# Kernel optimization log

Hardware: AMD Instinct MI355X
Metric: run time of the kernel (lower is better)

The kernel has to match this reference:

```python
import jax, jax.numpy as jnp
import numpy as np
from jax import lax

N, T, D_DYN = 3000, 64, 5
POP, DEMO, ECO, R = 16, 32, 16, 128
SLOPE = 0.01  # torch LeakyReLU default


def _leaky(x):
    return jnp.where(x >= 0, x, SLOPE * x)


def setup_inputs() -> dict:
    key = jax.random.key(0)
    ks = jax.random.split(key, 30)
    rn = lambda k, shape, s=0.1: (jax.random.normal(k, shape, jnp.float32) * s)
    inp = {
        "dynamic": jax.random.normal(ks[0], (N, T, D_DYN), jnp.float32),
        "pop": jax.random.normal(ks[1], (N, POP), jnp.float32),
        "demo": jax.random.normal(ks[2], (N, DEMO), jnp.float32),
        "eco": jax.random.normal(ks[3], (N, ECO), jnp.float32),
        "geo": jax.random.normal(ks[4], (N * N, 2), jnp.float32),
        # GAT-style static attention params
        "W_pop": rn(ks[5], (POP, POP)), "a_pop": rn(ks[6], (2 * POP, 1)),
        "W_demo": rn(ks[7], (DEMO, DEMO)), "a_demo": rn(ks[8], (2 * DEMO, 1)),
        "W_eco": rn(ks[9], (ECO, ECO)), "a_eco": rn(ks[10], (2 * ECO, 1)),
        "W_geo": rn(ks[11], (2, 2)), "a_geo": rn(ks[12], (2, 1)),
        # covid_weight MLP: 1 -> R -> 1
        "cw_w1": rn(ks[13], (1, R)), "cw_b1": rn(ks[14], (R,)),
        "cw_w2": rn(ks[15], (R, 1)), "cw_b2": rn(ks[16], (1,)),
        # hos_weight MLP: 4 -> R -> 4
        "hw_w1": rn(ks[17], (4, R)), "hw_b1": rn(ks[18], (R,)),
        "hw_w2": rn(ks[19], (R, 4)), "hw_b2": rn(ks[20], (4,)),
        # LSTM (torch gate order i,f,g,o), combined bias b_ih + b_hh
        "Wih": rn(ks[21], (D_DYN, 4 * R)), "Whh": rn(ks[22], (R, 4 * R)),
        "b_lstm": rn(ks[23], (4 * R,)),
        # output head
        "lin_w": rn(ks[24], (R, R)), "lin_b": rn(ks[25], (R,)),
        "lin2_w": rn(ks[26], (R, 1)), "lin2_b": rn(ks[27], (1,)),
    }
    return inp


def _pair_scores(x, W, a):
    # faithful to sigmoid(cat([h_i, h_j]) @ a): score[i,j] = h_i @ a1 + h_j @ a2
    h = x @ W                       # [N, D]
    d = W.shape[0]
    s1 = h @ a[:d, 0]               # [N]
    s2 = h @ a[d:, 0]               # [N]
    return jax.nn.sigmoid(s1[:, None] + s2[None, :])  # [N, N]


def _lstm(x, Wih, Whh, b):
    # x: [N, T, D_DYN] -> h_seq [N, T, R], (hT, cT)
    n = x.shape[0]
    h0 = jnp.zeros((n, R), x.dtype)
    c0 = jnp.zeros((n, R), x.dtype)

    def step(carry, xt):
        h, c = carry
        z = xt @ Wih + h @ Whh + b          # [N, 4R]
        i, f, g, o = jnp.split(z, 4, axis=-1)
        i, f, o = jax.nn.sigmoid(i), jax.nn.sigmoid(f), jax.nn.sigmoid(o)
        g = jnp.tanh(g)
        c = f * c + i * g
        h = o * jnp.tanh(c)
        return (h, c), h

    (hT, cT), hs = lax.scan(step, (h0, c0), x.transpose(1, 0, 2))
    return hs.transpose(1, 0, 2), hT, cT


def reference(dynamic, pop, demo, eco, geo,
              W_pop, a_pop, W_demo, a_demo, W_eco, a_eco, W_geo, a_geo,
              cw_w1, cw_b1, cw_w2, cw_b2, hw_w1, hw_b1, hw_w2, hw_b2,
              Wih, Whh, b_lstm, lin_w, lin_b, lin2_w, lin2_b):
    n, t = pop.shape[0], dynamic.shape[1]

    d_pop = _pair_scores(pop, W_pop, a_pop)
    d_demo = _pair_scores(demo, W_demo, a_demo)
    d_eco = _pair_scores(eco, W_eco, a_eco)
    d_geo = jax.nn.sigmoid(((geo @ W_geo) @ a_geo).reshape(n, n))

    dist = jax.nn.softmax(d_pop + d_demo + d_eco + d_geo, axis=-1)  # [N, N]

    cov_in = dynamic[:, :, 0:1]                                     # [N, T, 1]
    cov_w = jax.nn.sigmoid(_leaky(cov_in @ cw_w1 + cw_b1) @ cw_w2 + cw_b2)
    hos_in = dynamic[:, :, 1:5]                                     # [N, T, 4]
    hos_w = jax.nn.sigmoid(_leaky(hos_in @ hw_w1 + hw_b1) @ hw_w2 + hw_b2)
    total_weights = jnp.concatenate([cov_w, hos_w], axis=-1)        # [N, T, 5]

    h, hT, cT = _lstm(total_weights * dynamic, Wih, Whh, b_lstm)    # [N, T, R]

    # original: h + (h.reshape(N,1,T,R).repeat(1,N,1,1) * dist[:,:,None,None]).sum(1)
    # == h + h * dist.sum(axis=1) (h is broadcast along the summed axis)
    h_att = h + h * dist.sum(axis=1)[:, None, None]

    y = _leaky(h_att @ lin_w + lin_b) @ lin2_w + lin2_b             # [N, T, 1]
    return (y, dist, total_weights, hT, cT)
```

## Files before the change

kernel.cpp:

```cpp
#include <hip/hip_runtime.h>
#include <hip/hip_bf16.h>

#define N_NODES 3000
#define T_STEPS 64
#define POP     16
#define DEMO    32
#define ECO     16
#define R       128
#define SLOPE   0.01f

#define NBLK    250

#define WS_S1P 0
#define WS_S1D 3000
#define WS_S1E 6000
#define WS_S2P 9000
#define WS_S2D 12000
#define WS_S2E 15000
#define WS_GV  18000
#define WS_ATT 18432
#define WS_XW  21504
#define WS_PACK_F 981504

#define OUT_Y    0
#define OUT_DIST 192000
#define OUT_TW   9192000
#define OUT_HT   10152000
#define OUT_CT   10536000

typedef __bf16 bf16x8 __attribute__((ext_vector_type(8)));
typedef float  f32x4  __attribute__((ext_vector_type(4)));

__device__ __forceinline__ float sigf(float x) {
  return __builtin_amdgcn_rcpf(1.0f + __expf(-x));
}
__device__ __forceinline__ float leakyf(float x) { return x >= 0.0f ? x : SLOPE * x; }
__device__ __forceinline__ float tanhfast(float x) {
  return fmaf(-2.0f, __builtin_amdgcn_rcpf(__expf(2.0f * x) + 1.0f), 1.0f);
}
__device__ __forceinline__ unsigned short bfbits(float v) {
  __bf16 b = (__bf16)v;
  return __builtin_bit_cast(unsigned short, b);
}
template <int CTRL>
__device__ __forceinline__ float dppsum(float v) {
  int p = __builtin_amdgcn_update_dpp(0, __builtin_bit_cast(int, v), CTRL, 0xF, 0xF, true);
  return v + __builtin_bit_cast(float, p);
}

#define PIN4(x) { f32x4 _t = __builtin_bit_cast(f32x4, x); \
                  asm volatile("" : "+v"(_t)); \
                  x = __builtin_bit_cast(bf16x8, _t); }
#define PIN1(x) asm volatile("" : "+v"(x))

__global__ __launch_bounds__(256) void pack_kernel(
    const float* __restrict__ Whh, const float* __restrict__ lin_w,
    const float* __restrict__ Wih, const float* __restrict__ b_lstm,
    unsigned short* __restrict__ wsu)
{
  int idx = blockIdx.x * 256 + threadIdx.x;
  if (idx < 65536) {
    int i = idx & 7, lane = (idx >> 3) & 63, kc = (idx >> 9) & 3, ct = idx >> 11;
    int k = kc * 32 + ((lane >> 4) << 3) + i;
    int n = ct * 16 + (lane & 15);
    float v = Whh[k * 512 + n];
    float hi = (float)(__bf16)v;
    wsu[idx]         = bfbits(v);
    wsu[65536 + idx] = bfbits(v - hi);
  } else if (idx < 81920) {
    int q = idx - 65536;
    int i = q & 7, lane = (q >> 3) & 63, kc = (q >> 9) & 3, ct = q >> 11;
    int k = kc * 32 + ((lane >> 4) << 3) + i;
    int n = ct * 16 + (lane & 15);
    float v = lin_w[k * R + n];
    float hi = (float)(__bf16)v;
    wsu[131072 + q] = bfbits(v);
    wsu[147456 + q] = bfbits(v - hi);
  } else {
    int q = idx - 81920;
    int i = q & 7, lane = (q >> 3) & 63, ct = q >> 9;
    int ks = ((lane >> 4) << 3) + i;
    int n = ct * 16 + (lane & 15);
    unsigned short o = 0;
    if (ks < 5) {
      o = bfbits(Wih[ks * 512 + n]);
    } else if (ks == 6) {
      float b = b_lstm[n];
      o = bfbits(b - (float)(__bf16)b);
    } else if (ks == 7) {
      o = bfbits(b_lstm[n]);
    }
    wsu[163840 + q] = o;
  }
}

__global__ __launch_bounds__(256) void scores_kernel(
    const float* __restrict__ pop,  const float* __restrict__ demo,
    const float* __restrict__ eco,
    const float* __restrict__ W_pop,  const float* __restrict__ a_pop,
    const float* __restrict__ W_demo, const float* __restrict__ a_demo,
    const float* __restrict__ W_eco,  const float* __restrict__ a_eco,
    const float* __restrict__ W_geo,  const float* __restrict__ a_geo,
    float* __restrict__ ws)
{
  int i = blockIdx.x * blockDim.x + threadIdx.x;
  if (i == 0) {
    float a0 = a_geo[0], a1 = a_geo[1];
    ws[WS_GV + 0] = W_geo[0] * a0 + W_geo[1] * a1;
    ws[WS_GV + 1] = W_geo[2] * a0 + W_geo[3] * a1;
  }
  if (i >= N_NODES) return;
  {
    float x[POP];
#pragma unroll
    for (int k = 0; k < POP; k++) x[k] = pop[i * POP + k];
    float s1 = 0.f, s2 = 0.f;
#pragma unroll
    for (int r = 0; r < POP; r++) {
      float h = 0.f;
#pragma unroll
      for (int k = 0; k < POP; k++) h = fmaf(x[k], W_pop[k * POP + r], h);
      s1 = fmaf(h, a_pop[r], s1);
      s2 = fmaf(h, a_pop[POP + r], s2);
    }
    ws[WS_S1P + i] = s1; ws[WS_S2P + i] = s2;
  }
  {
    float x[DEMO];
#pragma unroll
    for (int k = 0; k < DEMO; k++) x[k] = demo[i * DEMO + k];
    float s1 = 0.f, s2 = 0.f;
#pragma unroll 4
    for (int r = 0; r < DEMO; r++) {
      float h = 0.f;
#pragma unroll
      for (int k = 0; k < DEMO; k++) h = fmaf(x[k], W_demo[k * DEMO + r], h);
      s1 = fmaf(h, a_demo[r], s1);
      s2 = fmaf(h, a_demo[DEMO + r], s2);
    }
    ws[WS_S1D + i] = s1; ws[WS_S2D + i] = s2;
  }
  {
    float x[ECO];
#pragma unroll
    for (int k = 0; k < ECO; k++) x[k] = eco[i * ECO + k];
    float s1 = 0.f, s2 = 0.f;
#pragma unroll
    for (int r = 0; r < ECO; r++) {
      float h = 0.f;
#pragma unroll
      for (int k = 0; k < ECO; k++) h = fmaf(x[k], W_eco[k * ECO + r], h);
      s1 = fmaf(h, a_eco[r], s1);
      s2 = fmaf(h, a_eco[ECO + r], s2);
    }
    ws[WS_S1E + i] = s1; ws[WS_S2E + i] = s2;
  }
}

__global__ __launch_bounds__(256) void weights_kernel(
    const float* __restrict__ dyn,
    const float* __restrict__ cw_w1, const float* __restrict__ cw_b1,
    const float* __restrict__ cw_w2, const float* __restrict__ cw_b2,
    const float* __restrict__ hw_w1, const float* __restrict__ hw_b1,
    const float* __restrict__ hw_w2, const float* __restrict__ hw_b2,
    float* __restrict__ out, float* __restrict__ ws)
{
  __shared__ float s_cw1[R], s_cb1[R], s_cw2[R], s_hb1[R];
  __shared__ float s_hw1[4 * R], s_hw2[R * 4];
  int tid = threadIdx.x;
  if (tid < R) {
    s_cw1[tid] = cw_w1[tid]; s_cb1[tid] = cw_b1[tid];
    s_cw2[tid] = cw_w2[tid]; s_hb1[tid] = hw_b1[tid];
  }
  for (int i = tid; i < 4 * R; i += 256) { s_hw1[i] = hw_w1[i]; s_hw2[i] = hw_w2[i]; }
  __syncthreads();

  int idx = blockIdx.x * 256 + tid;
  float x0 = dyn[idx * 5 + 0], x1 = dyn[idx * 5 + 1], x2 = dyn[idx * 5 + 2];
  float x3 = dyn[idx * 5 + 3], x4 = dyn[idx * 5 + 4];

  float acc = 0.f, o0 = 0.f, o1 = 0.f, o2 = 0.f, o3 = 0.f;
#pragma unroll 8
  for (int r = 0; r < R; r++) {
    float u = leakyf(fmaf(x0, s_cw1[r], s_cb1[r]));
    acc = fmaf(u, s_cw2[r], acc);
    float v = s_hb1[r];
    v = fmaf(x1, s_hw1[r], v);
    v = fmaf(x2, s_hw1[R + r], v);
    v = fmaf(x3, s_hw1[2 * R + r], v);
    v = fmaf(x4, s_hw1[3 * R + r], v);
    v = leakyf(v);
    o0 = fmaf(v, s_hw2[r * 4 + 0], o0);
    o1 = fmaf(v, s_hw2[r * 4 + 1], o1);
    o2 = fmaf(v, s_hw2[r * 4 + 2], o2);
    o3 = fmaf(v, s_hw2[r * 4 + 3], o3);
  }
  float tw0 = sigf(acc + cw_b2[0]);
  float tw1 = sigf(o0 + hw_b2[0]);
  float tw2 = sigf(o1 + hw_b2[1]);
  float tw3 = sigf(o2 + hw_b2[2]);
  float tw4 = sigf(o3 + hw_b2[3]);

  out[OUT_TW + idx * 5 + 0] = tw0;
  out[OUT_TW + idx * 5 + 1] = tw1;
  out[OUT_TW + idx * 5 + 2] = tw2;
  out[OUT_TW + idx * 5 + 3] = tw3;
  out[OUT_TW + idx * 5 + 4] = tw4;

  ws[WS_XW + idx * 5 + 0] = tw0 * x0;
  ws[WS_XW + idx * 5 + 1] = tw1 * x1;
  ws[WS_XW + idx * 5 + 2] = tw2 * x2;
  ws[WS_XW + idx * 5 + 3] = tw3 * x3;
  ws[WS_XW + idx * 5 + 4] = tw4 * x4;
}

__global__ __launch_bounds__(256) void dist_kernel(
    const float* __restrict__ geo, float* __restrict__ out, float* __restrict__ ws)
{
  int i = blockIdx.x;
  int tid = threadIdx.x;
  __shared__ float sm[20];

  float s1p = ws[WS_S1P + i], s1d = ws[WS_S1D + i], s1e = ws[WS_S1E + i];
  float gv0 = ws[WS_GV + 0], gv1 = ws[WS_GV + 1];

  float vals[12];
  float vmax = -3.0e38f;
#pragma unroll
  for (int u = 0; u < 12; u++) {
    int j = tid + u * 256;
    float v = -3.0e38f;
    if (j < N_NODES) {
      float2 g = *(const float2*)&geo[((size_t)i * N_NODES + j) * 2];
      v = sigf(s1p + ws[WS_S2P + j]) + sigf(s1d + ws[WS_S2D + j]) +
          sigf(s1e + ws[WS_S2E + j]) + sigf(fmaf(g.x, gv0, g.y * gv1));
    }
    vals[u] = v;
    vmax = fmaxf(vmax, v);
  }
  int wid = tid >> 6, lane = tid & 63;
  for (int off = 32; off; off >>= 1) vmax = fmaxf(vmax, __shfl_down(vmax, off, 64));
  if (lane == 0) sm[wid] = vmax;
  __syncthreads();
  if (tid == 0) sm[8] = fmaxf(fmaxf(sm[0], sm[1]), fmaxf(sm[2], sm[3]));
  __syncthreads();
  vmax = sm[8];

  float lsum = 0.f;
#pragma unroll
  for (int u = 0; u < 12; u++) {
    int j = tid + u * 256;
    float e = (j < N_NODES) ? __expf(vals[u] - vmax) : 0.f;
    vals[u] = e;
    lsum += e;
  }
  for (int off = 32; off; off >>= 1) lsum += __shfl_down(lsum, off, 64);
  if (lane == 0) sm[4 + wid] = lsum;
  __syncthreads();
  if (tid == 0) sm[9] = sm[4] + sm[5] + sm[6] + sm[7];
  __syncthreads();
  float inv = __builtin_amdgcn_rcpf(sm[9]);

  float rs = 0.f;
#pragma unroll
  for (int u = 0; u < 12; u++) {
    int j = tid + u * 256;
    if (j < N_NODES) {
      float wv = vals[u] * inv;
      out[OUT_DIST + (size_t)i * N_NODES + j] = wv;
      rs += wv;
    }
  }
  for (int off = 32; off; off >>= 1) rs += __shfl_down(rs, off, 64);
  if (lane == 0) sm[10 + wid] = rs;
  __syncthreads();
  if (tid == 0) ws[WS_ATT + i] = 1.0f + (sm[10] + sm[11] + sm[12] + sm[13]);
}

#define HB        6144
#define XWH       4096
#define XWL       5120
#define PART_OFF  12288
#define LDS_BYTES 13312

__global__ __launch_bounds__(512, 2) void lstm_kernel(
    const unsigned short* __restrict__ wsu,
    const float* __restrict__ ws,
    const float* __restrict__ lin_b, const float* __restrict__ lin2_w,
    const float* __restrict__ lin2_b,
    float* __restrict__ out)
{
  __shared__ __align__(16) char smraw[LDS_BYTES];
  float* PARTf = (float*)(smraw + PART_OFF);
  int tid = threadIdx.x;
  int w = tid >> 6, lane = tid & 63;
  int lg = lane >> 4, lc = lane & 15;
  int row0 = blockIdx.x * 12;

  bf16x8 bwh[4][4], bwl[4][4], bih[4], lh[4], ll[4];
#pragma unroll
  for (int g = 0; g < 4; g++) {
#pragma unroll
    for (int kc = 0; kc < 4; kc++) {
      int off = (((g * 8 + w) * 4 + kc) * 512) + lane * 8;
      bwh[g][kc] = *(const bf16x8*)(wsu + off);
      bwl[g][kc] = *(const bf16x8*)(wsu + 65536 + off);
      PIN4(bwh[g][kc]); PIN4(bwl[g][kc]);
    }
    bih[g] = *(const bf16x8*)(wsu + 163840 + (g * 8 + w) * 512 + lane * 8);
    PIN4(bih[g]);
  }
#pragma unroll
  for (int kc = 0; kc < 4; kc++) {
    int off = 131072 + (w * 4 + kc) * 512 + lane * 8;
    lh[kc] = *(const bf16x8*)(wsu + off);
    ll[kc] = *(const bf16x8*)(wsu + 16384 + off);
    PIN4(lh[kc]); PIN4(ll[kc]);
  }

  int hcol = w * 16 + lc;
  float lbv = lin_b[hcol], l2v = lin2_w[hcol], l2b = lin2_b[0];
  float sc[4];
#pragma unroll
  for (int j = 0; j < 4; j++) {
    int rg = row0 + lg * 4 + j; if (rg > 2999) rg = 2999;
    sc[j] = ws[WS_ATT + rg];
    PIN1(sc[j]);
  }
  PIN1(lbv); PIN1(l2v); PIN1(l2b);

  for (int p = tid; p < LDS_BYTES / 4; p += 512) ((float*)smraw)[p] = 0.f;
  __syncthreads();
  if (tid < 32) {
    int b = tid >> 4, r = tid & 15;
    *(unsigned short*)(smraw + b * HB + XWH + r * 16 + 12) = 0x3F80;
    *(unsigned short*)(smraw + b * HB + XWH + r * 16 + 14) = 0x3F80;
  }
  int pr = tid / 5, pd = tid - pr * 5;
  int prow = row0 + pr; if (prow > 2999) prow = 2999;
  const float* xw_row = ws + WS_XW + (size_t)prow * 320;
  if (tid < 80) {
    float v = xw_row[pd];
    float vh = (float)(__bf16)v;
    *(unsigned short*)(smraw + XWH + pr * 16 + pd * 2) = bfbits(v);
    *(unsigned short*)(smraw + XWL + pr * 16 + pd * 2) = bfbits(v - vh);
  }
  __syncthreads();

  int hi3 = (2 * w + (lc >> 3)) & 3;
  int hwbase = (w >> 1) * 1024 + hi3 * 256 + (lc & 7) * 2;

  bf16x8 ah[4];
  f32x4 zf4 = {0.f, 0.f, 0.f, 0.f};
#pragma unroll
  for (int kc = 0; kc < 4; kc++) ah[kc] = __builtin_bit_cast(bf16x8, zf4);
  float cst[4] = {0.f, 0.f, 0.f, 0.f};
  float val[4] = {0.f, 0.f, 0.f, 0.f};

#pragma unroll 1
  for (int t = 0; t < T_STEPS; t++) {
    char* bufcur = smraw + (t & 1) * HB;
    char* bufnxt = smraw + ((t & 1) ^ 1) * HB;

    float xnext = 0.f;
    if (tid < 80) {
      int tn = t + 1 < T_STEPS ? t + 1 : T_STEPS - 1;
      xnext = xw_row[tn * 5 + pd];
    }

    if (t > 0) {
#pragma unroll
      for (int j = 0; j < 4; j++) {
        float v = val[j];
        v = dppsum<0xB1>(v);
        v = dppsum<0x4E>(v);
        v = dppsum<0x141>(v);
        v = dppsum<0x140>(v);
        if (lc == 0) PARTf[((t - 1) & 1) * 128 + (lg * 4 + j) * 8 + w] = v;
      }
    }

    bf16x8 a4h = *(const bf16x8*)(bufcur + XWH + lane * 16);
    bf16x8 a4l = *(const bf16x8*)(bufcur + XWL + lane * 16);
    f32x4 acc[4];
#pragma unroll
    for (int g = 0; g < 4; g++) acc[g] = zf4;
#pragma unroll
    for (int kc = 0; kc < 4; kc++) {
#pragma unroll
      for (int g = 0; g < 4; g++)
        acc[g] = __builtin_amdgcn_mfma_f32_16x16x32_bf16(ah[kc], bwh[g][kc], acc[g], 0, 0, 0);
#pragma unroll
      for (int g = 0; g < 4; g++)
        acc[g] = __builtin_amdgcn_mfma_f32_16x16x32_bf16(ah[kc], bwl[g][kc], acc[g], 0, 0, 0);
    }
#pragma unroll
    for (int g = 0; g < 4; g++)
      acc[g] = __builtin_amdgcn_mfma_f32_16x16x32_bf16(a4h, bih[g], acc[g], 0, 0, 0);
#pragma unroll
    for (int g = 0; g < 4; g++)
      acc[g] = __builtin_amdgcn_mfma_f32_16x16x32_bf16(a4l, bih[g], acc[g], 0, 0, 0);

    float hval[4];
#pragma unroll
    for (int j = 0; j < 4; j++) {
      float ig = sigf(acc[0][j]), fg = sigf(acc[1][j]);
      float gg = tanhfast(acc[2][j]), og = sigf(acc[3][j]);
      float cn = fmaf(fg, cst[j], ig * gg);
      float hn = og * tanhfast(cn);
      cst[j] = cn; hval[j] = hn;
      *(unsigned short*)(bufcur + hwbase + (lg * 4 + j) * 16) = bfbits(hn);
    }
    if (tid < 80) {
      float vh = (float)(__bf16)xnext;
      *(unsigned short*)(bufnxt + XWH + pr * 16 + pd * 2) = bfbits(xnext);
      *(unsigned short*)(bufnxt + XWL + pr * 16 + pd * 2) = bfbits(xnext - vh);
    }
    if (t == T_STEPS - 1) {
#pragma unroll
      for (int j = 0; j < 4; j++) {
        int r = lg * 4 + j;
        if (r < 12) {
          out[OUT_HT + (size_t)(row0 + r) * R + hcol] = hval[j];
          out[OUT_CT + (size_t)(row0 + r) * R + hcol] = cst[j];
        }
      }
    }
    __syncthreads();

    if (t > 0 && tid < 12) {
      const float* pp = PARTf + ((t - 1) & 1) * 128 + tid * 8;
      float s = l2b;
#pragma unroll
      for (int p = 0; p < 8; p++) s += pp[p];
      out[OUT_Y + (size_t)(row0 + tid) * T_STEPS + (t - 1)] = s;
    }

#pragma unroll
    for (int kc = 0; kc < 4; kc++)
      ah[kc] = *(const bf16x8*)(bufcur + kc * 1024 + lane * 16);
    f32x4 ga = zf4, gb = zf4;
    ga = __builtin_amdgcn_mfma_f32_16x16x32_bf16(ah[0], lh[0], ga, 0, 0, 0);
    ga = __builtin_amdgcn_mfma_f32_16x16x32_bf16(ah[0], ll[0], ga, 0, 0, 0);
    ga = __builtin_amdgcn_mfma_f32_16x16x32_bf16(ah[1], lh[1], ga, 0, 0, 0);
    ga = __builtin_amdgcn_mfma_f32_16x16x32_bf16(ah[1], ll[1], ga, 0, 0, 0);
    gb = __builtin_amdgcn_mfma_f32_16x16x32_bf16(ah[2], lh[2], gb, 0, 0, 0);
    gb = __builtin_amdgcn_mfma_f32_16x16x32_bf16(ah[2], ll[2], gb, 0, 0, 0);
    gb = __builtin_amdgcn_mfma_f32_16x16x32_bf16(ah[3], lh[3], gb, 0, 0, 0);
    gb = __builtin_amdgcn_mfma_f32_16x16x32_bf16(ah[3], ll[3], gb, 0, 0, 0);
#pragma unroll
    for (int j = 0; j < 4; j++)
      val[j] = leakyf(fmaf(sc[j], ga[j] + gb[j], lbv)) * l2v;
  }

#pragma unroll
  for (int j = 0; j < 4; j++) {
    float v = val[j];
    v = dppsum<0xB1>(v); v = dppsum<0x4E>(v);
    v = dppsum<0x141>(v); v = dppsum<0x140>(v);
    if (lc == 0) PARTf[128 + (lg * 4 + j) * 8 + w] = v;
  }
  __syncthreads();
  if (tid < 12) {
    const float* pp = PARTf + 128 + tid * 8;
    float s = l2b;
#pragma unroll
    for (int p = 0; p < 8; p++) s += pp[p];
    out[OUT_Y + (size_t)(row0 + tid) * T_STEPS + 63] = s;
  }
}

extern "C" void kernel_launch(void* const* d_in, const int* in_sizes, int n_in,
                              void* d_out, int out_size, void* d_ws, size_t ws_size,
                              hipStream_t stream) {
  const float* dynamic = (const float*)d_in[0];
  const float* pop     = (const float*)d_in[1];
  const float* demo    = (const float*)d_in[2];
  const float* eco     = (const float*)d_in[3];
  const float* geo     = (const float*)d_in[4];
  const float* W_pop   = (const float*)d_in[5];
  const float* a_pop   = (const float*)d_in[6];
  const float* W_demo  = (const float*)d_in[7];
  const float* a_demo  = (const float*)d_in[8];
  const float* W_eco   = (const float*)d_in[9];
  const float* a_eco   = (const float*)d_in[10];
  const float* W_geo   = (const float*)d_in[11];
  const float* a_geo   = (const float*)d_in[12];
  const float* cw_w1   = (const float*)d_in[13];
  const float* cw_b1   = (const float*)d_in[14];
  const float* cw_w2   = (const float*)d_in[15];
  const float* cw_b2   = (const float*)d_in[16];
  const float* hw_w1   = (const float*)d_in[17];
  const float* hw_b1   = (const float*)d_in[18];
  const float* hw_w2   = (const float*)d_in[19];
  const float* hw_b2   = (const float*)d_in[20];
  const float* Wih     = (const float*)d_in[21];
  const float* Whh     = (const float*)d_in[22];
  const float* b_lstm  = (const float*)d_in[23];
  const float* lin_w   = (const float*)d_in[24];
  const float* lin_b   = (const float*)d_in[25];
  const float* lin2_w  = (const float*)d_in[26];
  const float* lin2_b  = (const float*)d_in[27];

  float* out = (float*)d_out;
  float* ws  = (float*)d_ws;
  unsigned short* wsu = (unsigned short*)(ws + WS_PACK_F);

  pack_kernel<<<384, 256, 0, stream>>>(Whh, lin_w, Wih, b_lstm, wsu);
  scores_kernel<<<12, 256, 0, stream>>>(pop, demo, eco, W_pop, a_pop,
                                        W_demo, a_demo, W_eco, a_eco,
                                        W_geo, a_geo, ws);
  weights_kernel<<<750, 256, 0, stream>>>(dynamic, cw_w1, cw_b1, cw_w2, cw_b2,
                                          hw_w1, hw_b1, hw_w2, hw_b2, out, ws);
  dist_kernel<<<N_NODES, 256, 0, stream>>>(geo, out, ws);
  lstm_kernel<<<NBLK, 512, 0, stream>>>(wsu, ws, lin_b, lin2_w, lin2_b, out);
}
```

Before: 311.9 us.

## Stream LSTM weights from L1/L2 each step and halve rows per block

The LSTM weight fragments are no longer held pinned in registers. They are repacked into a per-wave contiguous layout and reloaded from global memory (expected to hit in cache) on every timestep. This frees VGPRs, so the launch bound rises to 4 blocks per CU. Blocks now take 6 rows instead of 12, doubling the block count to 500 so all CUs can be filled. The cost is extra load traffic and latency inside the serial recurrence, and the MFMA tile still processes 16 rows while only 6 are valid, which wastes compute.

```diff
diff --git a/kernel.cpp b/kernel.cpp
--- a/kernel.cpp
+++ b/kernel.cpp
@@ -9,7 +9,8 @@
 #define R       128
 #define SLOPE   0.01f
 
-#define NBLK    250
+#define ROWS_PB 6
+#define NBLK    500
 
 #define WS_S1P 0
 #define WS_S1D 3000
@@ -47,10 +48,6 @@
   int p = __builtin_amdgcn_update_dpp(0, __builtin_bit_cast(int, v), CTRL, 0xF, 0xF, true);
   return v + __builtin_bit_cast(float, p);
 }
-
-#define PIN4(x) { f32x4 _t = __builtin_bit_cast(f32x4, x); \
-                  asm volatile("" : "+v"(_t)); \
-                  x = __builtin_bit_cast(bf16x8, _t); }
 #define PIN1(x) asm volatile("" : "+v"(x))
 
 __global__ __launch_bounds__(256) void pack_kernel(
@@ -59,39 +56,38 @@
     unsigned short* __restrict__ wsu)
 {
   int idx = blockIdx.x * 256 + threadIdx.x;
-  if (idx < 65536) {
-    int i = idx & 7, lane = (idx >> 3) & 63, kc = (idx >> 9) & 3, ct = idx >> 11;
-    int k = kc * 32 + ((lane >> 4) << 3) + i;
-    int n = ct * 16 + (lane & 15);
+  int i    = idx & 7;
+  int t1   = idx >> 3;
+  int lane = t1 & 63;
+  int t2   = t1 >> 6;
+  int f    = t2 % 44;
+  int w    = t2 / 44;
+
+  int ks = ((lane >> 4) << 3) + i;
+  int nc = lane & 15;
+  unsigned short o = 0;
+
+  if (f < 32) {
+    int kc = f >> 3, hl = (f >> 2) & 1, g = f & 3;
+    int k = kc * 32 + ks;
+    int n = g * 128 + w * 16 + nc;
     float v = Whh[k * 512 + n];
-    float hi = (float)(__bf16)v;
-    wsu[idx]         = bfbits(v);
-    wsu[65536 + idx] = bfbits(v - hi);
-  } else if (idx < 81920) {
-    int q = idx - 65536;
-    int i = q & 7, lane = (q >> 3) & 63, kc = (q >> 9) & 3, ct = q >> 11;
-    int k = kc * 32 + ((lane >> 4) << 3) + i;
-    int n = ct * 16 + (lane & 15);
+    o = hl ? bfbits(v - (float)(__bf16)v) : bfbits(v);
+  } else if (f < 36) {
+    int g = f - 32;
+    int n = g * 128 + w * 16 + nc;
+    if (ks < 5)      o = bfbits(Wih[ks * 512 + n]);
+    else if (ks == 6) { float b = b_lstm[n]; o = bfbits(b - (float)(__bf16)b); }
+    else if (ks == 7) o = bfbits(b_lstm[n]);
+  } else {
+    int q = f - 36;
+    int kc = q >> 1, hl = q & 1;
+    int k = kc * 32 + ks;
+    int n = w * 16 + nc;
     float v = lin_w[k * R + n];
-    float hi = (float)(__bf16)v;
-    wsu[131072 + q] = bfbits(v);
-    wsu[147456 + q] = bfbits(v - hi);
-  } else {
-    int q = idx - 81920;
-    int i = q & 7, lane = (q >> 3) & 63, ct = q >> 9;
-    int ks = ((lane >> 4) << 3) + i;
-    int n = ct * 16 + (lane & 15);
-    unsigned short o = 0;
-    if (ks < 5) {
-      o = bfbits(Wih[ks * 512 + n]);
-    } else if (ks == 6) {
-      float b = b_lstm[n];
-      o = bfbits(b - (float)(__bf16)b);
-    } else if (ks == 7) {
-      o = bfbits(b_lstm[n]);
-    }
-    wsu[163840 + q] = o;
-  }
+    o = hl ? bfbits(v - (float)(__bf16)v) : bfbits(v);
+  }
+  wsu[idx] = o;
 }
 
 __global__ __launch_bounds__(256) void scores_kernel(
@@ -282,8 +278,9 @@
 #define XWL       5120
 #define PART_OFF  12288
 #define LDS_BYTES 13312
-
-__global__ __launch_bounds__(512, 2) void lstm_kernel(
+#define WGRP_B    45056
+
+__global__ __launch_bounds__(512, 4) void lstm_kernel(
     const unsigned short* __restrict__ wsu,
     const float* __restrict__ ws,
     const float* __restrict__ lin_b, const float* __restrict__ lin2_w,
@@ -295,28 +292,9 @@
   int tid = threadIdx.x;
   int w = tid >> 6, lane = tid & 63;
   int lg = lane >> 4, lc = lane & 15;
-  int row0 = blockIdx.x * 12;
-
-  bf16x8 bwh[4][4], bwl[4][4], bih[4], lh[4], ll[4];
-#pragma unroll
-  for (int g = 0; g < 4; g++) {
-#pragma unroll
-    for (int kc = 0; kc < 4; kc++) {
-      int off = (((g * 8 + w) * 4 + kc) * 512) + lane * 8;
-      bwh[g][kc] = *(const bf16x8*)(wsu + off);
-      bwl[g][kc] = *(const bf16x8*)(wsu + 65536 + off);
-      PIN4(bwh[g][kc]); PIN4(bwl[g][kc]);
-    }
-    bih[g] = *(const bf16x8*)(wsu + 163840 + (g * 8 + w) * 512 + lane * 8);
-    PIN4(bih[g]);
-  }
-#pragma unroll
-  for (int kc = 0; kc < 4; kc++) {
-    int off = 131072 + (w * 4 + kc) * 512 + lane * 8;
-    lh[kc] = *(const bf16x8*)(wsu + off);
-    ll[kc] = *(const bf16x8*)(wsu + 16384 + off);
-    PIN4(lh[kc]); PIN4(ll[kc]);
-  }
+  int row0 = blockIdx.x * ROWS_PB;
+
+  const char* wb = (const char*)wsu + w * WGRP_B + lane * 16;
 
   int hcol = w * 16 + lc;
   float lbv = lin_b[hcol], l2v = lin2_w[hcol], l2b = lin2_b[0];
@@ -372,10 +350,8 @@
 #pragma unroll
       for (int j = 0; j < 4; j++) {
         float v = val[j];
-        v = dppsum<0xB1>(v);
-        v = dppsum<0x4E>(v);
-        v = dppsum<0x141>(v);
-        v = dppsum<0x140>(v);
+        v = dppsum<0xB1>(v); v = dppsum<0x4E>(v);
+        v = dppsum<0x141>(v); v = dppsum<0x140>(v);
         if (lc == 0) PARTf[((t - 1) & 1) * 128 + (lg * 4 + j) * 8 + w] = v;
       }
     }
@@ -387,19 +363,37 @@
     for (int g = 0; g < 4; g++) acc[g] = zf4;
 #pragma unroll
     for (int kc = 0; kc < 4; kc++) {
-#pragma unroll
-      for (int g = 0; g < 4; g++)
-        acc[g] = __builtin_amdgcn_mfma_f32_16x16x32_bf16(ah[kc], bwh[g][kc], acc[g], 0, 0, 0);
-#pragma unroll
-      for (int g = 0; g < 4; g++)
-        acc[g] = __builtin_amdgcn_mfma_f32_16x16x32_bf16(ah[kc], bwl[g][kc], acc[g], 0, 0, 0);
-    }
-#pragma unroll
-    for (int g = 0; g < 4; g++)
-      acc[g] = __builtin_amdgcn_mfma_f32_16x16x32_bf16(a4h, bih[g], acc[g], 0, 0, 0);
-#pragma unroll
-    for (int g = 0; g < 4; g++)
-      acc[g] = __builtin_amdgcn_mfma_f32_16x16x32_bf16(a4l, bih[g], acc[g], 0, 0, 0);
+      bf16x8 b0 = *(const bf16x8*)(wb + (kc * 8 + 0) * 1024);
+      bf16x8 b1 = *(const bf16x8*)(wb + (kc * 8 + 1) * 1024);
+      bf16x8 b2 = *(const bf16x8*)(wb + (kc * 8 + 2) * 1024);
+      bf16x8 b3 = *(const bf16x8*)(wb + (kc * 8 + 3) * 1024);
+      bf16x8 b4 = *(const bf16x8*)(wb + (kc * 8 + 4) * 1024);
+      bf16x8 b5 = *(const bf16x8*)(wb + (kc * 8 + 5) * 1024);
+      bf16x8 b6 = *(const bf16x8*)(wb + (kc * 8 + 6) * 1024);
+      bf16x8 b7 = *(const bf16x8*)(wb + (kc * 8 + 7) * 1024);
+      acc[0] = __builtin_amdgcn_mfma_f32_16x16x32_bf16(ah[kc], b0, acc[0], 0, 0, 0);
+      acc[1] = __builtin_amdgcn_mfma_f32_16x16x32_bf16(ah[kc], b1, acc[1], 0, 0, 0);
+      acc[2] = __builtin_amdgcn_mfma_f32_16x16x32_bf16(ah[kc], b2, acc[2], 0, 0, 0);
+      acc[3] = __builtin_amdgcn_mfma_f32_16x16x32_bf16(ah[kc], b3, acc[3], 0, 0, 0);
+      acc[0] = __builtin_amdgcn_mfma_f32_16x16x32_bf16(ah[kc], b4, acc[0], 0, 0, 0);
+      acc[1] = __builtin_amdgcn_mfma_f32_16x16x32_bf16(ah[kc], b5, acc[1], 0, 0, 0);
+      acc[2] = __builtin_amdgcn_mfma_f32_16x16x32_bf16(ah[kc], b6, acc[2], 0, 0, 0);
+      acc[3] = __builtin_amdgcn_mfma_f32_16x16x32_bf16(ah[kc], b7, acc[3], 0, 0, 0);
+    }
+    {
+      bf16x8 c0 = *(const bf16x8*)(wb + 32 * 1024);
+      bf16x8 c1 = *(const bf16x8*)(wb + 33 * 1024);
+      bf16x8 c2 = *(const bf16x8*)(wb + 34 * 1024);
+      bf16x8 c3 = *(const bf16x8*)(wb + 35 * 1024);
+      acc[0] = __builtin_amdgcn_mfma_f32_16x16x32_bf16(a4h, c0, acc[0], 0, 0, 0);
+      acc[1] = __builtin_amdgcn_mfma_f32_16x16x32_bf16(a4h, c1, acc[1], 0, 0, 0);
+      acc[2] = __builtin_amdgcn_mfma_f32_16x16x32_bf16(a4h, c2, acc[2], 0, 0, 0);
+      acc[3] = __builtin_amdgcn_mfma_f32_16x16x32_bf16(a4h, c3, acc[3], 0, 0, 0);
+      acc[0] = __builtin_amdgcn_mfma_f32_16x16x32_bf16(a4l, c0, acc[0], 0, 0, 0);
+      acc[1] = __builtin_amdgcn_mfma_f32_16x16x32_bf16(a4l, c1, acc[1], 0, 0, 0);
+      acc[2] = __builtin_amdgcn_mfma_f32_16x16x32_bf16(a4l, c2, acc[2], 0, 0, 0);
+      acc[3] = __builtin_amdgcn_mfma_f32_16x16x32_bf16(a4l, c3, acc[3], 0, 0, 0);
+    }
 
     float hval[4];
 #pragma unroll
@@ -411,6 +405,16 @@
       cst[j] = cn; hval[j] = hn;
       *(unsigned short*)(bufcur + hwbase + (lg * 4 + j) * 16) = bfbits(hn);
     }
+
+    bf16x8 p0 = *(const bf16x8*)(wb + 36 * 1024);
+    bf16x8 p1 = *(const bf16x8*)(wb + 37 * 1024);
+    bf16x8 p2 = *(const bf16x8*)(wb + 38 * 1024);
+    bf16x8 p3 = *(const bf16x8*)(wb + 39 * 1024);
+    bf16x8 p4 = *(const bf16x8*)(wb + 40 * 1024);
+    bf16x8 p5 = *(const bf16x8*)(wb + 41 * 1024);
+    bf16x8 p6 = *(const bf16x8*)(wb + 42 * 1024);
+    bf16x8 p7 = *(const bf16x8*)(wb + 43 * 1024);
+
     if (tid < 80) {
       float vh = (float)(__bf16)xnext;
       *(unsigned short*)(bufnxt + XWH + pr * 16 + pd * 2) = bfbits(xnext);
@@ -420,7 +424,7 @@
 #pragma unroll
       for (int j = 0; j < 4; j++) {
         int r = lg * 4 + j;
-        if (r < 12) {
+        if (r < ROWS_PB) {
           out[OUT_HT + (size_t)(row0 + r) * R + hcol] = hval[j];
           out[OUT_CT + (size_t)(row0 + r) * R + hcol] = cst[j];
         }
@@ -428,7 +432,7 @@
     }
     __syncthreads();
 
-    if (t > 0 && tid < 12) {
+    if (t > 0 && tid < ROWS_PB) {
       const float* pp = PARTf + ((t - 1) & 1) * 128 + tid * 8;
       float s = l2b;
 #pragma unroll
@@ -440,14 +444,14 @@
     for (int kc = 0; kc < 4; kc++)
       ah[kc] = *(const bf16x8*)(bufcur + kc * 1024 + lane * 16);
     f32x4 ga = zf4, gb = zf4;
-    ga = __builtin_amdgcn_mfma_f32_16x16x32_bf16(ah[0], lh[0], ga, 0, 0, 0);
-    ga = __builtin_amdgcn_mfma_f32_16x16x32_bf16(ah[0], ll[0], ga, 0, 0, 0);
-    ga = __builtin_amdgcn_mfma_f32_16x16x32_bf16(ah[1], lh[1], ga, 0, 0, 0);
-    ga = __builtin_amdgcn_mfma_f32_16x16x32_bf16(ah[1], ll[1], ga, 0, 0, 0);
-    gb = __builtin_amdgcn_mfma_f32_16x16x32_bf16(ah[2], lh[2], gb, 0, 0, 0);
-    gb = __builtin_amdgcn_mfma_f32_16x16x32_bf16(ah[2], ll[2], gb, 0, 0, 0);
-    gb = __builtin_amdgcn_mfma_f32_16x16x32_bf16(ah[3], lh[3], gb, 0, 0, 0);
-    gb = __builtin_amdgcn_mfma_f32_16x16x32_bf16(ah[3], ll[3], gb, 0, 0, 0);
+    ga = __builtin_amdgcn_mfma_f32_16x16x32_bf16(ah[0], p0, ga, 0, 0, 0);
+    ga = __builtin_amdgcn_mfma_f32_16x16x32_bf16(ah[0], p1, ga, 0, 0, 0);
+    ga = __builtin_amdgcn_mfma_f32_16x16x32_bf16(ah[1], p2, ga, 0, 0, 0);
+    ga = __builtin_amdgcn_mfma_f32_16x16x32_bf16(ah[1], p3, ga, 0, 0, 0);
+    gb = __builtin_amdgcn_mfma_f32_16x16x32_bf16(ah[2], p4, gb, 0, 0, 0);
+    gb = __builtin_amdgcn_mfma_f32_16x16x32_bf16(ah[2], p5, gb, 0, 0, 0);
+    gb = __builtin_amdgcn_mfma_f32_16x16x32_bf16(ah[3], p6, gb, 0, 0, 0);
+    gb = __builtin_amdgcn_mfma_f32_16x16x32_bf16(ah[3], p7, gb, 0, 0, 0);
 #pragma unroll
     for (int j = 0; j < 4; j++)
       val[j] = leakyf(fmaf(sc[j], ga[j] + gb[j], lbv)) * l2v;
@@ -461,7 +465,7 @@
     if (lc == 0) PARTf[128 + (lg * 4 + j) * 8 + w] = v;
   }
   __syncthreads();
-  if (tid < 12) {
+  if (tid < ROWS_PB) {
     const float* pp = PARTf + 128 + tid * 8;
     float s = l2b;
 #pragma unroll
@@ -506,7 +510,7 @@
   float* ws  = (float*)d_ws;
   unsigned short* wsu = (unsigned short*)(ws + WS_PACK_F);
 
-  pack_kernel<<<384, 256, 0, stream>>>(Whh, lin_w, Wih, b_lstm, wsu);
+  pack_kernel<<<704, 256, 0, stream>>>(Whh, lin_w, Wih, b_lstm, wsu);
   scores_kernel<<<12, 256, 0, stream>>>(pop, demo, eco, W_pop, a_pop,
                                         W_demo, a_demo, W_eco, a_eco,
                                         W_geo, a_geo, ws);
```

Measured after the change: 1.200 ms. +284.5%, slower.
